# Performance work log

Measured on AMD Instinct MI355X. Metric: run time of the kernel, lower is better.

## Reference

```python
import jax, jax.numpy as jnp
import numpy as np

EMB = 1024
HEADS = 16
HEAD_DIM = EMB // HEADS


def setup_inputs() -> dict:
    key = jax.random.key(0)
    ks = jax.random.split(key, 5)
    x = jax.random.normal(ks[0], (4, 2048, EMB), dtype=jnp.float32)
    # qkv Linear: weight [3*EMB, EMB] in torch; store transposed for x @ W
    Wqkv = jax.random.normal(ks[1], (EMB, 3 * EMB), dtype=jnp.float32) * (1.0 / np.sqrt(EMB))
    bqkv = jax.random.normal(ks[2], (3 * EMB,), dtype=jnp.float32) * 0.01
    Wout = jax.random.normal(ks[3], (EMB, EMB), dtype=jnp.float32) * (1.0 / np.sqrt(EMB))
    bout = jax.random.normal(ks[4], (EMB,), dtype=jnp.float32) * 0.01
    return {"x": x, "Wqkv": Wqkv, "bqkv": bqkv, "Wout": Wout, "bout": bout}


def reference(x, Wqkv, bqkv, Wout, bout):
    B, N, _ = x.shape
    qkv = x @ Wqkv + bqkv                              # [B, N, 3*EMB]
    qkv = qkv.reshape(B, N, 3, HEADS, HEAD_DIM)
    q, k, v = jnp.moveaxis(qkv, 2, 0)                  # each [B, N, H, D]
    q = jnp.swapaxes(q, 1, 2)                          # [B, H, N, D]
    k = jnp.swapaxes(k, 1, 2)
    v = jnp.swapaxes(v, 1, 2)
    scale = 1.0 / np.sqrt(HEAD_DIM).astype(np.float32)
    scores = jnp.einsum('bhqd,bhkd->bhqk', q, k) * scale
    attn = jax.nn.softmax(scores, axis=-1)             # dropout p=0 (eval)
    out = jnp.einsum('bhqk,bhkd->bhqd', attn, v)       # [B, H, N, D]
    out = jnp.swapaxes(out, 1, 2).reshape(B, N, EMB)
    return out @ Wout + bout
```

## Files before the change

kernel.cpp:

```cpp
#include <hip/hip_runtime.h>

#define SEQ   2048
#define EMBD  1024
#define HEADS 16
#define HDIM  64
#define MTOT  8192

typedef __attribute__((ext_vector_type(8))) _Float16 half8;
typedef __attribute__((ext_vector_type(4))) _Float16 half4;
typedef __attribute__((ext_vector_type(2))) __fp16 fp16x2;
typedef __attribute__((ext_vector_type(4))) float f32x4;
typedef __attribute__((ext_vector_type(16))) float f32x16;

__device__ __forceinline__ f32x4 mfma16(half8 a, half8 b, f32x4 c) {
  return __builtin_amdgcn_mfma_f32_16x16x32_f16(a, b, c, 0, 0, 0);
}
__device__ __forceinline__ f32x16 mfma32(half8 a, half8 b, f32x16 c) {
  return __builtin_amdgcn_mfma_f32_32x32x16_f16(a, b, c, 0, 0, 0);
}

__device__ __forceinline__ void gload_lds16(const void* g, void* l) {
  __builtin_amdgcn_global_load_lds(
      (const __attribute__((address_space(1))) unsigned int*)g,
      (__attribute__((address_space(3))) unsigned int*)l, 16, 0, 0);
}

__device__ __forceinline__ unsigned pk2(float a, float b) {
  union { fp16x2 v; unsigned u; } t;
  t.v = __builtin_amdgcn_cvt_pkrtz(a, b);
  return t.u;
}

__global__ void k_cvt(const float* __restrict__ in, _Float16* __restrict__ out) {
  size_t i = (size_t)blockIdx.x * blockDim.x + threadIdx.x;
  const f32x4* in4 = (const f32x4*)in;
  f32x4 a = in4[2 * i], b = in4[2 * i + 1];
  half8 h;
  h[0] = (_Float16)a[0]; h[1] = (_Float16)a[1];
  h[2] = (_Float16)a[2]; h[3] = (_Float16)a[3];
  h[4] = (_Float16)b[0]; h[5] = (_Float16)b[1];
  h[6] = (_Float16)b[2]; h[7] = (_Float16)b[3];
  *(half8*)(out + i * 8) = h;
}

__global__ __launch_bounds__(256) void k_transpose(const float* __restrict__ in,
                                                   _Float16* __restrict__ out,
                                                   int R, int C) {
  __shared__ _Float16 tile[64][65];
  const int tid = threadIdx.x;
  const int r0 = blockIdx.y * 64, c0 = blockIdx.x * 64;
  const int tr = tid >> 6;
  const int tc = tid & 63;
  #pragma unroll
  for (int i = 0; i < 16; ++i) {
    const int r = i * 4 + tr;
    tile[r][tc] = (_Float16)in[(size_t)(r0 + r) * C + c0 + tc];
  }
  __syncthreads();
  #pragma unroll
  for (int i = 0; i < 16; ++i) {
    const int cc = i * 4 + tr;
    out[(size_t)(c0 + cc) * R + r0 + tc] = tile[tc][cc];
  }
}

template<int EPI>
__global__ __launch_bounds__(256) void k_gemm(
    const _Float16* __restrict__ A, const _Float16* __restrict__ Bt,
    const float* __restrict__ bias, float* __restrict__ outf,
    _Float16* __restrict__ q, _Float16* __restrict__ k, _Float16* __restrict__ vt)
{
  __shared__ _Float16 sm[128 * 132];
  _Float16* sA = sm;
  _Float16* sB = sm + 128 * 64;
  const int tid = threadIdx.x;
  const int l = tid & 63, g = l >> 4, c = l & 15;
  const int w = tid >> 6;
  const int wm = (w >> 1) * 64, wn = (w & 1) * 64;
  const int rowBase = blockIdx.y * 128;
  const int colBase = blockIdx.x * 128;

  f32x4 acc[4][4] = {};

  const _Float16* Ag = A + (size_t)(rowBase + (tid >> 3)) * 1024 + (tid & 7) * 8;
  const _Float16* Bg = Bt + (size_t)(colBase + (tid >> 3)) * 1024 + (tid & 7) * 8;
  _Float16* la = sA + tid * 8;
  _Float16* lb = sB + tid * 8;

  for (int kt = 0; kt < 16; ++kt) {
    const _Float16* ag = Ag + kt * 64;
    const _Float16* bg = Bg + kt * 64;
    #pragma unroll
    for (int i = 0; i < 4; ++i) {
      gload_lds16(ag + (size_t)i * 32 * 1024, la + i * 256 * 8);
      gload_lds16(bg + (size_t)i * 32 * 1024, lb + i * 256 * 8);
    }
    __syncthreads();
    #pragma unroll
    for (int kk = 0; kk < 2; ++kk) {
      half8 af[4], bf[4];
      #pragma unroll
      for (int t = 0; t < 4; ++t)
        af[t] = *(const half8*)(sA + (wm + t * 16 + c) * 64 + kk * 32 + g * 8);
      #pragma unroll
      for (int t = 0; t < 4; ++t)
        bf[t] = *(const half8*)(sB + (wn + t * 16 + c) * 64 + kk * 32 + g * 8);
      #pragma unroll
      for (int mt = 0; mt < 4; ++mt)
        #pragma unroll
        for (int nt = 0; nt < 4; ++nt)
          acc[mt][nt] = mfma16(af[mt], bf[nt], acc[mt][nt]);
    }
    __syncthreads();
  }

  if constexpr (EPI == 0) {
    if (colBase >= 2048) {
      __syncthreads();
      #pragma unroll
      for (int nt = 0; nt < 4; ++nt) {
        const int col_l = wn + nt * 16 + c;
        const float bv = bias[colBase + col_l];
        #pragma unroll
        for (int mt = 0; mt < 4; ++mt) {
          half4 hv;
          hv[0] = (_Float16)(acc[mt][nt][0] + bv);
          hv[1] = (_Float16)(acc[mt][nt][1] + bv);
          hv[2] = (_Float16)(acc[mt][nt][2] + bv);
          hv[3] = (_Float16)(acc[mt][nt][3] + bv);
          *(half4*)(sm + col_l * 132 + wm + mt * 16 + g * 4) = hv;
        }
      }
      __syncthreads();
      const int b = rowBase >> 11;
      const int col = colBase + (tid >> 1);
      const int h = (col >> 6) & 15, d = col & 63;
      _Float16* dst = vt + ((size_t)(b * HEADS + h) * HDIM + d) * SEQ +
                      (rowBase & 2047) + (tid & 1) * 64;
      const _Float16* src = sm + (tid >> 1) * 132 + (tid & 1) * 64;
      #pragma unroll
      for (int j = 0; j < 8; ++j)
        *(half8*)(dst + j * 8) = *(const half8*)(src + j * 8);
    } else {
      #pragma unroll
      for (int mt = 0; mt < 4; ++mt) {
        #pragma unroll
        for (int nt = 0; nt < 4; ++nt) {
          const int col = colBase + wn + nt * 16 + c;
          const float bv = bias[col];
          const int s = col >> 10, h = (col >> 6) & 15, d = col & 63;
          #pragma unroll
          for (int r = 0; r < 4; ++r) {
            const int row = rowBase + wm + mt * 16 + g * 4 + r;
            const int b = row >> 11, n = row & 2047;
            const _Float16 hv = (_Float16)(acc[mt][nt][r] + bv);
            _Float16* dst = s ? k : q;
            dst[((size_t)(b * HEADS + h) * SEQ + n) * HDIM + d] = hv;
          }
        }
      }
    }
  } else {
    #pragma unroll
    for (int mt = 0; mt < 4; ++mt)
      #pragma unroll
      for (int nt = 0; nt < 4; ++nt) {
        const int col = colBase + wn + nt * 16 + c;
        const float bv = bias[col];
        #pragma unroll
        for (int r = 0; r < 4; ++r) {
          const int row = rowBase + wm + mt * 16 + g * 4 + r;
          outf[(size_t)row * EMBD + col] = acc[mt][nt][r] + bv;
        }
      }
  }
}

__global__ __launch_bounds__(512, 4) void k_attn(
    const _Float16* __restrict__ q, const _Float16* __restrict__ kg,
    const _Float16* __restrict__ vt, _Float16* __restrict__ aout)
{
  __shared__ _Float16 sm[128 * 72 + 64 * 136 + 8 * 32 * 76];
  _Float16* Ks = sm;
  _Float16* Vs = sm + 128 * 72;
  const int tid = threadIdx.x;
  const int w = tid >> 6, l = tid & 63;
  const int q32 = l & 31;
  const int hi = l >> 5;
  const bool hib = hi != 0;

  const int orig = blockIdx.x;
  const int lb = (orig & 7) * 64 + (orig >> 3);
  const int bh = lb >> 3;
  const int n0 = (lb & 7) * 256 + w * 32;

  const _Float16* qb = q  + (size_t)bh * SEQ * HDIM;
  const _Float16* kb = kg + (size_t)bh * SEQ * HDIM;
  const _Float16* vb = vt + (size_t)bh * HDIM * SEQ;
  const int row0 = tid >> 3, cb = tid & 7;

  const _Float16 qs = (_Float16)(0.125f * 1.44269504f);
  half8 aq[4];
  #pragma unroll
  for (int ch = 0; ch < 4; ++ch) {
    half8 t = *(const half8*)(qb + (size_t)(n0 + q32) * HDIM + ch * 16 + hi * 8);
    aq[ch] = t * qs;
  }

  float l_ = 0.f;
  f32x16 o0 = {}, o1 = {};

  half8 kr0 = *(const half8*)(kb + (size_t)tid * 8);
  half8 kr1 = *(const half8*)(kb + 4096 + (size_t)tid * 8);
  half8 vr0 = *(const half8*)(vb + (size_t)row0 * SEQ + cb * 8);
  half8 vr1 = *(const half8*)(vb + (size_t)row0 * SEQ + 64 + cb * 8);

  for (int kt = 0; kt < SEQ / 128; ++kt) {
    __syncthreads();
    *(half8*)(Ks + row0 * 72 + cb * 8) = kr0;
    *(half8*)(Ks + (row0 + 64) * 72 + cb * 8) = kr1;
    *(half8*)(Vs + row0 * 136 + cb * 8) = vr0;
    *(half8*)(Vs + row0 * 136 + 64 + cb * 8) = vr1;
    if (kt + 1 < SEQ / 128) {
      const _Float16* kn = kb + (size_t)(kt + 1) * 128 * HDIM;
      kr0 = *(const half8*)(kn + (size_t)tid * 8);
      kr1 = *(const half8*)(kn + 4096 + (size_t)tid * 8);
      const _Float16* vn = vb + (size_t)row0 * SEQ + (kt + 1) * 128;
      vr0 = *(const half8*)(vn + cb * 8);
      vr1 = *(const half8*)(vn + 64 + cb * 8);
    }
    __syncthreads();

    #pragma unroll
    for (int p = 0; p < 2; ++p) {
      f32x16 s0 = {}, s1 = {};
      __builtin_amdgcn_s_setprio(1);
      #pragma unroll
      for (int ch = 0; ch < 4; ++ch) {
        half8 ak0 = *(const half8*)(Ks + (p * 64 + q32) * 72 + ch * 16 + hi * 8);
        half8 ak1 = *(const half8*)(Ks + (p * 64 + 32 + q32) * 72 + ch * 16 + hi * 8);
        s0 = mfma32(ak0, aq[ch], s0);
        s1 = mfma32(ak1, aq[ch], s1);
      }
      __builtin_amdgcn_s_setprio(0);

      float pe[32];
      #pragma unroll
      for (int e = 0; e < 16; ++e) {
        pe[e]      = __builtin_amdgcn_exp2f(s0[e] - 8.0f);
        pe[16 + e] = __builtin_amdgcn_exp2f(s1[e] - 8.0f);
      }
      {
        float ts[8];
        #pragma unroll
        for (int i = 0; i < 8; ++i)
          ts[i] = (pe[i] + pe[i + 8]) + (pe[i + 16] + pe[i + 24]);
        l_ += ((ts[0] + ts[1]) + (ts[2] + ts[3])) +
              ((ts[4] + ts[5]) + (ts[6] + ts[7]));
      }

      __builtin_amdgcn_s_setprio(1);
      #pragma unroll
      for (int ch = 0; ch < 4; ++ch) {
        const int bs = ch * 8;
        unsigned A0 = pk2(pe[bs + 0], pe[bs + 1]);
        unsigned A1 = pk2(pe[bs + 2], pe[bs + 3]);
        unsigned B0 = pk2(pe[bs + 4], pe[bs + 5]);
        unsigned B1 = pk2(pe[bs + 6], pe[bs + 7]);
        unsigned F0 = hib ? A0 : B0;
        unsigned F1 = hib ? A1 : B1;
        unsigned xF0 = __shfl_xor(F0, 32, 64);
        unsigned xF1 = __shfl_xor(F1, 32, 64);
        union { unsigned u[4]; half8 h; } fr;
        fr.u[0] = hib ? xF0 : A0;
        fr.u[1] = hib ? xF1 : A1;
        fr.u[2] = hib ? B0 : xF0;
        fr.u[3] = hib ? B1 : xF1;
        half8 av0 = *(const half8*)(Vs + q32 * 136 + p * 64 + ch * 16 + hi * 8);
        half8 av1 = *(const half8*)(Vs + (32 + q32) * 136 + p * 64 + ch * 16 + hi * 8);
        o0 = mfma32(av0, fr.h, o0);
        o1 = mfma32(av1, fr.h, o1);
      }
      __builtin_amdgcn_s_setprio(0);
    }
  }

  const float lt = l_ + __shfl_xor(l_, 32, 64);
  const float rl = __builtin_amdgcn_rcpf(lt);

  _Float16* Ot = sm + 128 * 72 + 64 * 136 + w * 32 * 76;
  #pragma unroll
  for (int dh = 0; dh < 2; ++dh) {
    #pragma unroll
    for (int j = 0; j < 4; ++j) {
      union { unsigned u[2]; half4 h; } t;
      if (dh == 0) {
        t.u[0] = pk2(o0[4 * j] * rl, o0[4 * j + 1] * rl);
        t.u[1] = pk2(o0[4 * j + 2] * rl, o0[4 * j + 3] * rl);
      } else {
        t.u[0] = pk2(o1[4 * j] * rl, o1[4 * j + 1] * rl);
        t.u[1] = pk2(o1[4 * j + 2] * rl, o1[4 * j + 3] * rl);
      }
      *(half4*)(Ot + q32 * 76 + dh * 32 + 8 * j + 4 * hi) = t.h;
    }
  }

  const int b = bh >> 4, h = bh & 15;
  #pragma unroll
  for (int i = 0; i < 4; ++i) {
    const int qq = 8 * i + (l >> 3);
    half8 v = *(const half8*)(Ot + qq * 76 + (l & 7) * 8);
    *(half8*)(aout + (size_t)(b * SEQ + n0 + qq) * EMBD + h * HDIM + (l & 7) * 8) = v;
  }
}

extern "C" void kernel_launch(void* const* d_in, const int* in_sizes, int n_in,
                              void* d_out, int out_size, void* d_ws, size_t ws_size,
                              hipStream_t stream) {
  const float* x    = (const float*)d_in[0];
  const float* Wqkv = (const float*)d_in[1];
  const float* bqkv = (const float*)d_in[2];
  const float* Wout = (const float*)d_in[3];
  const float* bout = (const float*)d_in[4];
  float* out = (float*)d_out;

  _Float16* ws    = (_Float16*)d_ws;
  _Float16* xh    = ws;
  _Float16* wqkvt = xh + (size_t)MTOT * EMBD;
  _Float16* woutt = wqkvt + (size_t)3 * EMBD * EMBD;
  _Float16* qbuf  = woutt + (size_t)EMBD * EMBD;
  _Float16* kbuf  = qbuf + (size_t)MTOT * EMBD;
  _Float16* vtbuf = kbuf + (size_t)MTOT * EMBD;
  _Float16* aout  = xh;

  k_cvt<<<4096, 256, 0, stream>>>(x, xh);
  k_transpose<<<dim3(48, 16), 256, 0, stream>>>(Wqkv, wqkvt, 1024, 3072);
  k_transpose<<<dim3(16, 16), 256, 0, stream>>>(Wout, woutt, 1024, 1024);
  k_gemm<0><<<dim3(24, 64), 256, 0, stream>>>(xh, wqkvt, bqkv, nullptr,
                                              qbuf, kbuf, vtbuf);
  k_attn<<<512, 512, 0, stream>>>(qbuf, kbuf, vtbuf, aout);
  k_gemm<1><<<dim3(8, 64), 256, 0, stream>>>(aout, woutt, bout, out,
                                             nullptr, nullptr, nullptr);
}
```

Baseline: 218.3 us.

## Double-buffer K/V tiles in LDS to halve barriers in attention loop

The attention kernel now keeps two LDS buffers for K and V tiles. Each iteration writes the next tile into the spare buffer and prefetches the tile after that from global memory into registers, with one barrier per iteration instead of two. This hides LDS store latency and cuts synchronisation, but doubles the K/V shared memory footprint (about 70 KB), which may lower occupancy below the requested 4 blocks of 512 threads per CU. The output staging buffer reuses the start of shared memory after the final barrier.

```diff
diff --git a/kernel.cpp b/kernel.cpp
--- a/kernel.cpp
+++ b/kernel.cpp
@@ -180,9 +180,7 @@
     const _Float16* __restrict__ q, const _Float16* __restrict__ kg,
     const _Float16* __restrict__ vt, _Float16* __restrict__ aout)
 {
-  __shared__ _Float16 sm[128 * 72 + 64 * 136 + 8 * 32 * 76];
-  _Float16* Ks = sm;
-  _Float16* Vs = sm + 128 * 72;
+  __shared__ _Float16 sm[2 * (128 * 72 + 64 * 136)];
   const int tid = threadIdx.x;
   const int w = tid >> 6, l = tid & 63;
   const int q32 = l & 31;
@@ -214,22 +212,40 @@
   half8 kr1 = *(const half8*)(kb + 4096 + (size_t)tid * 8);
   half8 vr0 = *(const half8*)(vb + (size_t)row0 * SEQ + cb * 8);
   half8 vr1 = *(const half8*)(vb + (size_t)row0 * SEQ + 64 + cb * 8);
+  {
+    _Float16* K0 = sm;
+    _Float16* V0 = sm + 128 * 72;
+    *(half8*)(K0 + row0 * 72 + cb * 8) = kr0;
+    *(half8*)(K0 + (row0 + 64) * 72 + cb * 8) = kr1;
+    *(half8*)(V0 + row0 * 136 + cb * 8) = vr0;
+    *(half8*)(V0 + row0 * 136 + 64 + cb * 8) = vr1;
+  }
+  kr0 = *(const half8*)(kb + 128 * HDIM + (size_t)tid * 8);
+  kr1 = *(const half8*)(kb + 128 * HDIM + 4096 + (size_t)tid * 8);
+  vr0 = *(const half8*)(vb + (size_t)row0 * SEQ + 128 + cb * 8);
+  vr1 = *(const half8*)(vb + (size_t)row0 * SEQ + 192 + cb * 8);
+  __syncthreads();
 
   for (int kt = 0; kt < SEQ / 128; ++kt) {
-    __syncthreads();
-    *(half8*)(Ks + row0 * 72 + cb * 8) = kr0;
-    *(half8*)(Ks + (row0 + 64) * 72 + cb * 8) = kr1;
-    *(half8*)(Vs + row0 * 136 + cb * 8) = vr0;
-    *(half8*)(Vs + row0 * 136 + 64 + cb * 8) = vr1;
+    _Float16* Kc = sm + (kt & 1) * 17920;
+    _Float16* Vc = Kc + 128 * 72;
+    _Float16* Kn = sm + ((kt & 1) ^ 1) * 17920;
+    _Float16* Vn = Kn + 128 * 72;
+
     if (kt + 1 < SEQ / 128) {
-      const _Float16* kn = kb + (size_t)(kt + 1) * 128 * HDIM;
+      *(half8*)(Kn + row0 * 72 + cb * 8) = kr0;
+      *(half8*)(Kn + (row0 + 64) * 72 + cb * 8) = kr1;
+      *(half8*)(Vn + row0 * 136 + cb * 8) = vr0;
+      *(half8*)(Vn + row0 * 136 + 64 + cb * 8) = vr1;
+    }
+    if (kt + 2 < SEQ / 128) {
+      const _Float16* kn = kb + (size_t)(kt + 2) * 128 * HDIM;
       kr0 = *(const half8*)(kn + (size_t)tid * 8);
       kr1 = *(const half8*)(kn + 4096 + (size_t)tid * 8);
-      const _Float16* vn = vb + (size_t)row0 * SEQ + (kt + 1) * 128;
+      const _Float16* vn = vb + (size_t)row0 * SEQ + (kt + 2) * 128;
       vr0 = *(const half8*)(vn + cb * 8);
       vr1 = *(const half8*)(vn + 64 + cb * 8);
     }
-    __syncthreads();
 
     #pragma unroll
     for (int p = 0; p < 2; ++p) {
@@ -237,8 +253,8 @@
       __builtin_amdgcn_s_setprio(1);
       #pragma unroll
       for (int ch = 0; ch < 4; ++ch) {
-        half8 ak0 = *(const half8*)(Ks + (p * 64 + q32) * 72 + ch * 16 + hi * 8);
-        half8 ak1 = *(const half8*)(Ks + (p * 64 + 32 + q32) * 72 + ch * 16 + hi * 8);
+        half8 ak0 = *(const half8*)(Kc + (p * 64 + q32) * 72 + ch * 16 + hi * 8);
+        half8 ak1 = *(const half8*)(Kc + (p * 64 + 32 + q32) * 72 + ch * 16 + hi * 8);
         s0 = mfma32(ak0, aq[ch], s0);
         s1 = mfma32(ak1, aq[ch], s1);
       }
@@ -276,19 +292,20 @@
         fr.u[1] = hib ? xF1 : A1;
         fr.u[2] = hib ? B0 : xF0;
         fr.u[3] = hib ? B1 : xF1;
-        half8 av0 = *(const half8*)(Vs + q32 * 136 + p * 64 + ch * 16 + hi * 8);
-        half8 av1 = *(const half8*)(Vs + (32 + q32) * 136 + p * 64 + ch * 16 + hi * 8);
+        half8 av0 = *(const half8*)(Vc + q32 * 136 + p * 64 + ch * 16 + hi * 8);
+        half8 av1 = *(const half8*)(Vc + (32 + q32) * 136 + p * 64 + ch * 16 + hi * 8);
         o0 = mfma32(av0, fr.h, o0);
         o1 = mfma32(av1, fr.h, o1);
       }
       __builtin_amdgcn_s_setprio(0);
     }
+    __syncthreads();
   }
 
   const float lt = l_ + __shfl_xor(l_, 32, 64);
   const float rl = __builtin_amdgcn_rcpf(lt);
 
-  _Float16* Ot = sm + 128 * 72 + 64 * 136 + w * 32 * 76;
+  _Float16* Ot = sm + w * 32 * 76;
   #pragma unroll
   for (int dh = 0; dh < 2; ++dh) {
     #pragma unroll
```

Result: slower. 605.8 us (+177.5%).
